# Optimization experiments

Hardware: AMD Instinct MI355X
Metric: run time of the kernel (lower is better)

The kernel has to match this reference:

```python
import jax, jax.numpy as jnp
import numpy as np

DELTA_VAR = 1.0
DELTA_DIST = 2.0
VAR_W = 1.0
DIST_W = 1.0
REG_W = 1.0


def _per_sample_loss(X, L, K, delta_reg):
    # X: [N, d] embeddings, L: [N] int cluster ids in [0, K)
    N, d = X.shape
    ind = (L[None, :] == jnp.arange(K)[:, None]).astype(X.dtype)  # [K, N]
    sizes = ind.sum(axis=1)                                       # [K]
    centers = (ind @ X) / sizes[:, None]                          # [K, d]
    # distance of each point to each cluster center: [K, N]
    dist = jnp.sqrt(((X[None, :, :] - centers[:, None, :]) ** 2).sum(axis=2))
    err = jnp.clip(dist - DELTA_VAR, 0.0) ** 2
    var_terms = (ind * err).sum(axis=1) / sizes                   # [K]
    var_term = var_terms.mean()
    # pairwise center distances: [K, K]
    dmat = jnp.sqrt(((centers[None, :, :] - centers[:, None, :]) ** 2).sum(axis=2))
    eye = jnp.eye(K, dtype=X.dtype)
    dist_cost = jnp.clip(DELTA_DIST - (dmat + eye * DELTA_DIST), 0.0) ** 2
    dist_term = dist_cost.sum() / (K * (K - 1))
    center_norms = jnp.sqrt((centers ** 2).sum(axis=1))
    reg_term = (jnp.clip(center_norms - delta_reg, 0.0) ** 2).mean()
    return var_term, dist_term, reg_term


def setup_inputs() -> dict:
    key = jax.random.key(0)
    k1, k2 = jax.random.split(key)
    B, d, H, W, K = 8, 16, 512, 512, 8
    data = jax.random.normal(k1, (B, d, H, W), dtype=jnp.float32)
    labels = jax.random.randint(k2, (B, H, W), 0, K, dtype=jnp.int64)
    return {"data": data, "labels": labels, "n_clusters": K}


def reference(data, labels, n_clusters):
    B, d, H, W = data.shape
    delta_reg = jnp.sqrt(jnp.asarray(d, dtype=data.dtype))
    X = data.reshape(B, d, H * W).transpose(0, 2, 1)  # [B, N, d]
    L = labels.reshape(B, H * W)                      # [B, N]
    var_t, dist_t, reg_t = jax.vmap(
        lambda x, l: _per_sample_loss(x, l, n_clusters, delta_reg)
    )(X, L)
    loss = VAR_W * var_t.mean() + DIST_W * dist_t.mean() + REG_W * reg_t.mean()
    return loss
```

## Files before the change

kernel.cpp:

```cpp
#include <hip/hip_runtime.h>
#include <hip/hip_bf16.h>

#define BB 8
#define DD 16
#define KK 8
#define NN (512 * 512)
#define G4 (NN / 4)

constexpr int BPB   = 256;
constexpr int T     = 256;
constexpr int WV    = T / 64;
constexpr int WPB   = BPB * WV;
constexpr int SLOTS = WPB * 4;
constexpr int ITERS = G4 / SLOTS;

#define WS_SUMS    0
#define WS_CNTS    1024
#define WS_CENTERS 1088
#define WS_DISTREG 2112
#define WS_VARSUMS 2120
#define WS_TOTAL   2184

__device__ __forceinline__ float fcomp(const float4& v, int p) {
    switch (p) { case 0: return v.x; case 1: return v.y; case 2: return v.z; default: return v.w; }
}

__global__ __launch_bounds__(T, 8) void k_sums(const float* __restrict__ data,
                                               const int* __restrict__ labels,
                                               float* __restrict__ ws) {
    const int b    = blockIdx.x / BPB;
    const int blk  = blockIdx.x % BPB;
    const int tid  = threadIdx.x;
    const int wv   = tid >> 6;
    const int lane = tid & 63;
    const int d    = lane >> 2;
    const int r    = lane & 3;
    const int w    = blk * WV + wv;

    const float4* dp4 = (const float4*)(data + (size_t)b * DD * NN) + (size_t)d * G4;
    const int4*   lp4 = (const int4*)(labels + (size_t)b * NN);

    float s[KK], c[KK];
#pragma unroll
    for (int k = 0; k < KK; ++k) { s[k] = 0.f; c[k] = 0.f; }

#pragma unroll 4
    for (int i = 0; i < ITERS; ++i) {
        const int gg = i * SLOTS + w * 4 + r;
        float4 x  = dp4[gg];
        int4   lb = lp4[gg];
        int labs[4] = {lb.x, lb.y, lb.z, lb.w};
#pragma unroll
        for (int p = 0; p < 4; ++p) {
            float xv = fcomp(x, p);
            int   l  = labs[p];
#pragma unroll
            for (int k = 0; k < KK; ++k) {
                bool m = (l == k);
                s[k] += m ? xv : 0.0f;
                c[k] += m ? 1.0f : 0.0f;
            }
        }
    }

#pragma unroll
    for (int k = 0; k < KK; ++k) {
        s[k] += __shfl_xor(s[k], 1, 64);
        s[k] += __shfl_xor(s[k], 2, 64);
        c[k] += __shfl_xor(c[k], 1, 64);
        c[k] += __shfl_xor(c[k], 2, 64);
    }

    __shared__ float sred[WV][DD][KK];
    __shared__ float cred[WV][KK];
    if (r == 0) {
#pragma unroll
        for (int k = 0; k < KK; ++k) sred[wv][d][k] = s[k];
        if (d == 0) {
#pragma unroll
            for (int k = 0; k < KK; ++k) cred[wv][k] = c[k];
        }
    }
    __syncthreads();

    if (tid < DD * KK) {
        const int dd = tid >> 3, k = tid & 7;
        float v = 0.f;
#pragma unroll
        for (int ww = 0; ww < WV; ++ww) v += sred[ww][dd][k];
        atomicAdd(&ws[WS_SUMS + (b * KK + k) * DD + dd], v);
    }
    if (tid >= 128 && tid < 128 + KK) {
        const int k = tid - 128;
        float v = 0.f;
#pragma unroll
        for (int ww = 0; ww < WV; ++ww) v += cred[ww][k];
        atomicAdd(&ws[WS_CNTS + b * KK + k], v);
    }
}

__global__ void k_centers(float* __restrict__ ws) {
    const int t = threadIdx.x;
    const int b = t >> 3, k = t & 7;
    const float inv = 1.0f / ws[WS_CNTS + t];
    __shared__ float sc[BB * KK][DD];
    float cen[DD];
    float n2 = 0.f;
#pragma unroll
    for (int d = 0; d < DD; ++d) {
        float v = ws[WS_SUMS + t * DD + d] * inv;
        cen[d] = v;
        sc[t][d] = v;
        ws[WS_CENTERS + t * DD + d] = v;
        n2 = fmaf(v, v, n2);
    }
    __syncthreads();
    float rg = fmaxf(sqrtf(n2) - 4.0f, 0.f);
    rg *= rg;
    float rowcost = 0.f;
#pragma unroll
    for (int j = 0; j < KK; ++j) {
        float d2 = 0.f;
#pragma unroll
        for (int d = 0; d < DD; ++d) {
            float df = cen[d] - sc[b * KK + j][d];
            d2 = fmaf(df, df, d2);
        }
        float dm = sqrtf(d2) + ((j == k) ? 2.0f : 0.0f);
        float h = fmaxf(2.0f - dm, 0.f);
        rowcost += h * h;
    }
#pragma unroll
    for (int m = 1; m < 8; m <<= 1) {
        rowcost += __shfl_xor(rowcost, m, 64);
        rg      += __shfl_xor(rg, m, 64);
    }
    if (k == 0)
        ws[WS_DISTREG + b] = rowcost / (float)(KK * (KK - 1)) + rg / (float)KK;
}

__global__ __launch_bounds__(T, 8) void k_var(const float* __restrict__ data,
                                              const int* __restrict__ labels,
                                              float* __restrict__ ws) {
    const int b    = blockIdx.x / BPB;
    const int blk  = blockIdx.x % BPB;
    const int tid  = threadIdx.x;
    const int wv   = tid >> 6;
    const int lane = tid & 63;
    const int d    = lane >> 2;
    const int r    = lane & 3;
    const int w    = blk * WV + wv;

    __shared__ float cs[KK * DD];
    if (tid < KK * DD) cs[tid] = ws[WS_CENTERS + b * KK * DD + tid];
    __syncthreads();

    const float4* dp4 = (const float4*)(data + (size_t)b * DD * NN) + (size_t)d * G4;
    const int4*   lp4 = (const int4*)(labels + (size_t)b * NN);

    float acc[KK];
#pragma unroll
    for (int k = 0; k < KK; ++k) acc[k] = 0.f;

#pragma unroll 4
    for (int i = 0; i < ITERS; ++i) {
        const int gg = i * SLOTS + w * 4 + r;
        float4 x  = dp4[gg];
        int4   lb = lp4[gg];
        int labs[4] = {lb.x, lb.y, lb.z, lb.w};
#pragma unroll
        for (int p = 0; p < 4; ++p) {
            const int l = labs[p];
            float cv = cs[l * DD + d];
            float pd = fcomp(x, p) - cv;
            float ss = pd * pd;
            ss += __shfl_xor(ss, 4, 64);
            ss += __shfl_xor(ss, 8, 64);
            ss += __shfl_xor(ss, 16, 64);
            ss += __shfl_xor(ss, 32, 64);
            float e = fmaxf(sqrtf(ss) - 1.0f, 0.f);
            float e2 = e * e;
#pragma unroll
            for (int k = 0; k < KK; ++k) acc[k] += (l == k) ? e2 : 0.0f;
        }
    }

#pragma unroll
    for (int k = 0; k < KK; ++k) {
        acc[k] += __shfl_xor(acc[k], 1, 64);
        acc[k] += __shfl_xor(acc[k], 2, 64);
    }
    __shared__ float vred[WV][KK];
    if (lane == 0) {
#pragma unroll
        for (int k = 0; k < KK; ++k) vred[wv][k] = acc[k];
    }
    __syncthreads();
    if (tid < KK) {
        float v = 0.f;
#pragma unroll
        for (int ww = 0; ww < WV; ++ww) v += vred[ww][tid];
        atomicAdd(&ws[WS_VARSUMS + b * KK + tid], v);
    }
}

__global__ void k_final(const float* __restrict__ ws, float* __restrict__ out) {
    const int t = threadIdx.x;
    const int b = t >> 3;
    float v = ws[WS_VARSUMS + t] / ws[WS_CNTS + t];
#pragma unroll
    for (int m = 1; m < 8; m <<= 1) v += __shfl_xor(v, m, 64);
    float term = v / (float)KK + ws[WS_DISTREG + b];
#pragma unroll
    for (int m = 8; m < 64; m <<= 1) term += __shfl_xor(term, m, 64);
    if (t == 0) out[0] = term / (float)BB;
}

extern "C" void kernel_launch(void* const* d_in, const int* in_sizes, int n_in,
                              void* d_out, int out_size, void* d_ws, size_t ws_size,
                              hipStream_t stream) {
    const float* data   = (const float*)d_in[0];
    const int*   labels = (const int*)d_in[1];
    float*       ws     = (float*)d_ws;

    hipMemsetAsync(d_ws, 0, WS_TOTAL * sizeof(float), stream);
    k_sums<<<BB * BPB, T, 0, stream>>>(data, labels, ws);
    k_centers<<<1, 64, 0, stream>>>(ws);
    k_var<<<BB * BPB, T, 0, stream>>>(data, labels, ws);
    k_final<<<1, 64, 0, stream>>>(ws, (float*)d_out);
}
```

Measured before the change: 260.6 us.

## Restructure variance pass per-pixel, ballot counts, fold centers into final kernel

The sums kernel now has each thread cover two feature dims per loaded label vector, which halves label reloads, and counts labels with ballot/popcount instead of per-lane float adds. The variance kernel is rewritten so each thread owns four pixels and loops over all 16 dims, removing the per-point cross-lane shuffle reduction. Each block computes its centers inline from sums and counts. The separate centers kernel is removed and its work merged into the final kernel, which saves one launch. The trade-off is more per-thread serial work and fewer in-flight loads per thread in the variance pass.

```diff
diff --git a/kernel.cpp b/kernel.cpp
--- a/kernel.cpp
+++ b/kernel.cpp
@@ -7,23 +7,17 @@
 #define NN (512 * 512)
 #define G4 (NN / 4)
 
-constexpr int BPB   = 256;
-constexpr int T     = 256;
-constexpr int WV    = T / 64;
-constexpr int WPB   = BPB * WV;
-constexpr int SLOTS = WPB * 4;
-constexpr int ITERS = G4 / SLOTS;
+constexpr int BPB = 256;
+constexpr int T   = 256;
+constexpr int WV  = 4;
+constexpr int WPB = BPB * WV;
+constexpr int SL  = WPB * 8;
+constexpr int IT1 = G4 / SL;
 
 #define WS_SUMS    0
 #define WS_CNTS    1024
-#define WS_CENTERS 1088
-#define WS_DISTREG 2112
-#define WS_VARSUMS 2120
-#define WS_TOTAL   2184
-
-__device__ __forceinline__ float fcomp(const float4& v, int p) {
-    switch (p) { case 0: return v.x; case 1: return v.y; case 2: return v.z; default: return v.w; }
-}
+#define WS_VARSUMS 1088
+#define WS_TOTAL   1152
 
 __global__ __launch_bounds__(T, 8) void k_sums(const float* __restrict__ data,
                                                const int* __restrict__ labels,
@@ -33,53 +27,64 @@
     const int tid  = threadIdx.x;
     const int wv   = tid >> 6;
     const int lane = tid & 63;
-    const int d    = lane >> 2;
-    const int r    = lane & 3;
+    const int d8   = lane >> 3;
+    const int r8   = lane & 7;
     const int w    = blk * WV + wv;
 
-    const float4* dp4 = (const float4*)(data + (size_t)b * DD * NN) + (size_t)d * G4;
+    const float4* dlo = (const float4*)(data + (size_t)b * DD * NN) + (size_t)d8 * G4;
+    const float4* dhi = dlo + (size_t)8 * G4;
     const int4*   lp4 = (const int4*)(labels + (size_t)b * NN);
 
-    float s[KK], c[KK];
-#pragma unroll
-    for (int k = 0; k < KK; ++k) { s[k] = 0.f; c[k] = 0.f; }
-
-#pragma unroll 4
-    for (int i = 0; i < ITERS; ++i) {
-        const int gg = i * SLOTS + w * 4 + r;
-        float4 x  = dp4[gg];
-        int4   lb = lp4[gg];
-        int labs[4] = {lb.x, lb.y, lb.z, lb.w};
+    float slo[KK], shi[KK];
+    unsigned int cnt[KK];
+#pragma unroll
+    for (int k = 0; k < KK; ++k) { slo[k] = 0.f; shi[k] = 0.f; cnt[k] = 0u; }
+
+#pragma unroll 2
+    for (int i = 0; i < IT1; ++i) {
+        const int gg = i * SL + w * 8 + r8;
+        float4 xlo = dlo[gg];
+        float4 xhi = dhi[gg];
+        int4   lb  = lp4[gg];
+        int   labs[4] = {lb.x, lb.y, lb.z, lb.w};
+        float xl[4]   = {xlo.x, xlo.y, xlo.z, xlo.w};
+        float xh[4]   = {xhi.x, xhi.y, xhi.z, xhi.w};
 #pragma unroll
         for (int p = 0; p < 4; ++p) {
-            float xv = fcomp(x, p);
-            int   l  = labs[p];
+            const int   l = labs[p];
+            const float a = xl[p];
+            const float h = xh[p];
 #pragma unroll
             for (int k = 0; k < KK; ++k) {
                 bool m = (l == k);
-                s[k] += m ? xv : 0.0f;
-                c[k] += m ? 1.0f : 0.0f;
+                slo[k] += m ? a : 0.f;
+                shi[k] += m ? h : 0.f;
+                cnt[k] += (unsigned)__popcll(__ballot(m));
             }
         }
     }
 
 #pragma unroll
     for (int k = 0; k < KK; ++k) {
-        s[k] += __shfl_xor(s[k], 1, 64);
-        s[k] += __shfl_xor(s[k], 2, 64);
-        c[k] += __shfl_xor(c[k], 1, 64);
-        c[k] += __shfl_xor(c[k], 2, 64);
+#pragma unroll
+        for (int m = 1; m < 8; m <<= 1) {
+            slo[k] += __shfl_xor(slo[k], m, 64);
+            shi[k] += __shfl_xor(shi[k], m, 64);
+        }
     }
 
     __shared__ float sred[WV][DD][KK];
     __shared__ float cred[WV][KK];
-    if (r == 0) {
-#pragma unroll
-        for (int k = 0; k < KK; ++k) sred[wv][d][k] = s[k];
-        if (d == 0) {
-#pragma unroll
-            for (int k = 0; k < KK; ++k) cred[wv][k] = c[k];
-        }
+    if (r8 == 0) {
+#pragma unroll
+        for (int k = 0; k < KK; ++k) {
+            sred[wv][d8][k]     = slo[k];
+            sred[wv][d8 + 8][k] = shi[k];
+        }
+    }
+    if (lane == 0) {
+#pragma unroll
+        for (int k = 0; k < KK; ++k) cred[wv][k] = (float)(cnt[k] >> 3);
     }
     __syncthreads();
 
@@ -87,19 +92,82 @@
         const int dd = tid >> 3, k = tid & 7;
         float v = 0.f;
 #pragma unroll
-        for (int ww = 0; ww < WV; ++ww) v += sred[ww][dd][k];
+        for (int q = 0; q < WV; ++q) v += sred[q][dd][k];
         atomicAdd(&ws[WS_SUMS + (b * KK + k) * DD + dd], v);
-    }
-    if (tid >= 128 && tid < 128 + KK) {
-        const int k = tid - 128;
+    } else if (tid < DD * KK + KK) {
+        const int k = tid - DD * KK;
         float v = 0.f;
 #pragma unroll
-        for (int ww = 0; ww < WV; ++ww) v += cred[ww][k];
+        for (int q = 0; q < WV; ++q) v += cred[q][k];
         atomicAdd(&ws[WS_CNTS + b * KK + k], v);
     }
 }
 
-__global__ void k_centers(float* __restrict__ ws) {
+__global__ __launch_bounds__(T, 8) void k_var(const float* __restrict__ data,
+                                              const int* __restrict__ labels,
+                                              float* __restrict__ ws) {
+    const int b   = blockIdx.x / BPB;
+    const int blk = blockIdx.x % BPB;
+    const int tid = threadIdx.x;
+
+    __shared__ float cs[KK * 17 + DD];
+    if (tid < KK * DD) {
+        const int k = tid >> 4, d = tid & 15;
+        cs[k * 17 + d] = ws[WS_SUMS + (b * KK + k) * DD + d] / ws[WS_CNTS + b * KK + k];
+    }
+    __syncthreads();
+
+    const float4* dp4 = (const float4*)(data + (size_t)b * DD * NN);
+    const int4*   lp4 = (const int4*)(labels + (size_t)b * NN);
+    const int g = blk * T + tid;
+
+    int4 lb = lp4[g];
+    int labs[4] = {lb.x, lb.y, lb.z, lb.w};
+    float ss[4] = {0.f, 0.f, 0.f, 0.f};
+#pragma unroll 4
+    for (int d = 0; d < DD; ++d) {
+        float4 x = dp4[(size_t)d * G4 + g];
+        float xs[4] = {x.x, x.y, x.z, x.w};
+#pragma unroll
+        for (int p = 0; p < 4; ++p) {
+            float c  = cs[labs[p] * 17 + d];
+            float df = xs[p] - c;
+            ss[p] = fmaf(df, df, ss[p]);
+        }
+    }
+
+    float acc[KK];
+#pragma unroll
+    for (int k = 0; k < KK; ++k) acc[k] = 0.f;
+#pragma unroll
+    for (int p = 0; p < 4; ++p) {
+        float e  = fmaxf(sqrtf(ss[p]) - 1.0f, 0.f);
+        float e2 = e * e;
+#pragma unroll
+        for (int k = 0; k < KK; ++k) acc[k] += (labs[p] == k) ? e2 : 0.f;
+    }
+
+    const int lane = tid & 63, wv = tid >> 6;
+#pragma unroll
+    for (int k = 0; k < KK; ++k) {
+#pragma unroll
+        for (int m = 1; m < 64; m <<= 1) acc[k] += __shfl_xor(acc[k], m, 64);
+    }
+    __shared__ float vred[WV][KK];
+    if (lane == 0) {
+#pragma unroll
+        for (int k = 0; k < KK; ++k) vred[wv][k] = acc[k];
+    }
+    __syncthreads();
+    if (tid < KK) {
+        float v = 0.f;
+#pragma unroll
+        for (int q = 0; q < WV; ++q) v += vred[q][tid];
+        atomicAdd(&ws[WS_VARSUMS + b * KK + tid], v);
+    }
+}
+
+__global__ void k_final(const float* __restrict__ ws, float* __restrict__ out) {
     const int t = threadIdx.x;
     const int b = t >> 3, k = t & 7;
     const float inv = 1.0f / ws[WS_CNTS + t];
@@ -111,7 +179,6 @@
         float v = ws[WS_SUMS + t * DD + d] * inv;
         cen[d] = v;
         sc[t][d] = v;
-        ws[WS_CENTERS + t * DD + d] = v;
         n2 = fmaf(v, v, n2);
     }
     __syncthreads();
@@ -130,89 +197,10 @@
         float h = fmaxf(2.0f - dm, 0.f);
         rowcost += h * h;
     }
-#pragma unroll
-    for (int m = 1; m < 8; m <<= 1) {
-        rowcost += __shfl_xor(rowcost, m, 64);
-        rg      += __shfl_xor(rg, m, 64);
-    }
-    if (k == 0)
-        ws[WS_DISTREG + b] = rowcost / (float)(KK * (KK - 1)) + rg / (float)KK;
-}
-
-__global__ __launch_bounds__(T, 8) void k_var(const float* __restrict__ data,
-                                              const int* __restrict__ labels,
-                                              float* __restrict__ ws) {
-    const int b    = blockIdx.x / BPB;
-    const int blk  = blockIdx.x % BPB;
-    const int tid  = threadIdx.x;
-    const int wv   = tid >> 6;
-    const int lane = tid & 63;
-    const int d    = lane >> 2;
-    const int r    = lane & 3;
-    const int w    = blk * WV + wv;
-
-    __shared__ float cs[KK * DD];
-    if (tid < KK * DD) cs[tid] = ws[WS_CENTERS + b * KK * DD + tid];
-    __syncthreads();
-
-    const float4* dp4 = (const float4*)(data + (size_t)b * DD * NN) + (size_t)d * G4;
-    const int4*   lp4 = (const int4*)(labels + (size_t)b * NN);
-
-    float acc[KK];
-#pragma unroll
-    for (int k = 0; k < KK; ++k) acc[k] = 0.f;
-
-#pragma unroll 4
-    for (int i = 0; i < ITERS; ++i) {
-        const int gg = i * SLOTS + w * 4 + r;
-        float4 x  = dp4[gg];
-        int4   lb = lp4[gg];
-        int labs[4] = {lb.x, lb.y, lb.z, lb.w};
-#pragma unroll
-        for (int p = 0; p < 4; ++p) {
-            const int l = labs[p];
-            float cv = cs[l * DD + d];
-            float pd = fcomp(x, p) - cv;
-            float ss = pd * pd;
-            ss += __shfl_xor(ss, 4, 64);
-            ss += __shfl_xor(ss, 8, 64);
-            ss += __shfl_xor(ss, 16, 64);
-            ss += __shfl_xor(ss, 32, 64);
-            float e = fmaxf(sqrtf(ss) - 1.0f, 0.f);
-            float e2 = e * e;
-#pragma unroll
-            for (int k = 0; k < KK; ++k) acc[k] += (l == k) ? e2 : 0.0f;
-        }
-    }
-
-#pragma unroll
-    for (int k = 0; k < KK; ++k) {
-        acc[k] += __shfl_xor(acc[k], 1, 64);
-        acc[k] += __shfl_xor(acc[k], 2, 64);
-    }
-    __shared__ float vred[WV][KK];
-    if (lane == 0) {
-#pragma unroll
-        for (int k = 0; k < KK; ++k) vred[wv][k] = acc[k];
-    }
-    __syncthreads();
-    if (tid < KK) {
-        float v = 0.f;
-#pragma unroll
-        for (int ww = 0; ww < WV; ++ww) v += vred[ww][tid];
-        atomicAdd(&ws[WS_VARSUMS + b * KK + tid], v);
-    }
-}
-
-__global__ void k_final(const float* __restrict__ ws, float* __restrict__ out) {
-    const int t = threadIdx.x;
-    const int b = t >> 3;
-    float v = ws[WS_VARSUMS + t] / ws[WS_CNTS + t];
-#pragma unroll
-    for (int m = 1; m < 8; m <<= 1) v += __shfl_xor(v, m, 64);
-    float term = v / (float)KK + ws[WS_DISTREG + b];
-#pragma unroll
-    for (int m = 8; m < 64; m <<= 1) term += __shfl_xor(term, m, 64);
+    float var  = ws[WS_VARSUMS + t] * inv;
+    float term = var / (float)KK + rowcost / 56.0f + rg / (float)KK;
+#pragma unroll
+    for (int m = 1; m < 64; m <<= 1) term += __shfl_xor(term, m, 64);
     if (t == 0) out[0] = term / (float)BB;
 }
 
@@ -225,7 +213,6 @@
 
     hipMemsetAsync(d_ws, 0, WS_TOTAL * sizeof(float), stream);
     k_sums<<<BB * BPB, T, 0, stream>>>(data, labels, ws);
-    k_centers<<<1, 64, 0, stream>>>(ws);
     k_var<<<BB * BPB, T, 0, stream>>>(data, labels, ws);
     k_final<<<1, 64, 0, stream>>>(ws, (float*)d_out);
 }
```

New measurement: 237.2 us. -9.0%, faster.
